# Kernel tuning notes

Measured on AMD Instinct MI355X. Metric: run time of the kernel, lower is better.

Reference implementation:

```python
import jax, jax.numpy as jnp
import numpy as np

PAD_IDX = 0
VOCAB = 60
HIDDEN = 128
BATCH = 1024
SEQ = 256


def setup_inputs() -> dict:
    key = jax.random.key(0)
    ks = jax.random.split(key, 6)
    x = jax.random.randint(ks[0], (BATCH, SEQ), 0, VOCAB, dtype=jnp.int64 if jax.config.jax_enable_x64 else jnp.int32)
    lengths = jax.random.randint(ks[1], (BATCH,), 1, SEQ + 1, dtype=x.dtype)
    emb = jax.random.normal(ks[2], (VOCAB, HIDDEN), dtype=jnp.float32) * 0.1
    emb = emb.at[PAD_IDX].set(0.0)  # nn.Embedding padding_idx row is zero
    W_ih = jax.random.normal(ks[3], (HIDDEN, HIDDEN), dtype=jnp.float32) * (1.0 / np.sqrt(HIDDEN))
    W_hh = jax.random.normal(ks[4], (HIDDEN, HIDDEN), dtype=jnp.float32) * (1.0 / np.sqrt(HIDDEN))
    W_fc = jax.random.normal(ks[5], (VOCAB, HIDDEN), dtype=jnp.float32) * (1.0 / np.sqrt(HIDDEN))
    b_fc = jnp.zeros((VOCAB,), dtype=jnp.float32)
    return {"x": x, "lengths": lengths, "emb": emb, "W_ih": W_ih,
            "W_hh": W_hh, "W_fc": W_fc, "b_fc": b_fc}


def reference(x, lengths, emb, W_ih, W_hh, W_fc, b_fc):
    embedded = emb[x]                      # [B, T, H]
    B = embedded.shape[0]
    h0 = jnp.zeros((B, HIDDEN), dtype=embedded.dtype)

    def step(h_prev, x_t):
        # z_t = x_t @ W_ih^T + h_prev @ W_hh^T ; h_t = tanh(z_t)
        h_t = jnp.tanh(x_t @ W_ih.T + h_prev @ W_hh.T)
        return h_t, h_t

    _, hs = jax.lax.scan(step, h0, jnp.swapaxes(embedded, 0, 1))  # hs: [T, B, H]
    outputs = jnp.swapaxes(hs, 0, 1)       # [B, T, H]
    last_out = jnp.take_along_axis(outputs, (lengths - 1)[:, None, None], axis=1)[:, 0, :]  # [B, H]
    return last_out @ W_fc.T + b_fc[None, :]
```

## Files before the change

kernel.cpp:

```cpp
#include <hip/hip_runtime.h>
#include <hip/hip_bf16.h>

#define BATCH 1024
#define SEQ 256
#define HIDDEN 128
#define VOCAB 60
#define ROWS 4
#define ASTRIDE 144
#define XSTR (SEQ + 4)

typedef _Float16 f16x8 __attribute__((ext_vector_type(8)));
typedef float f32x4 __attribute__((ext_vector_type(4)));

__device__ __forceinline__ float fast_tanh(float x) {
    float e = __builtin_amdgcn_exp2f(x * 2.8853900817779268f);
    return __builtin_fmaf(-2.0f, __builtin_amdgcn_rcpf(e + 1.0f), 1.0f);
}

__device__ __forceinline__ f32x4 MF(f16x8 a, f16x8 b, f32x4 c) {
    return __builtin_amdgcn_mfma_f32_16x16x32_f16(a, b, c, 0, 0, 0);
}

__global__ void rnn_prep_embw(const float* __restrict__ emb,
                              const float* __restrict__ W_ih,
                              float* __restrict__ embW) {
    const int v = blockIdx.x;
    const int i = threadIdx.x;
    __shared__ __align__(16) float e[HIDDEN];
    e[i] = emb[v * HIDDEN + i];
    __syncthreads();
    const float4* wrow = (const float4*)(W_ih + i * HIDDEN);
    const float4* e4 = (const float4*)e;
    float a0 = 0.f, a1 = 0.f, a2 = 0.f, a3 = 0.f;
#pragma unroll
    for (int j = 0; j < HIDDEN / 4; ++j) {
        float4 w = wrow[j];
        float4 h = e4[j];
        a0 += w.x * h.x; a1 += w.y * h.y; a2 += w.z * h.z; a3 += w.w * h.w;
    }
    embW[v * HIDDEN + i] = (a0 + a1) + (a2 + a3);
}

__global__ void __launch_bounds__(256)
rnn_mfma(const int* __restrict__ x, const int* __restrict__ lengths,
         const float* __restrict__ embW, const float* __restrict__ W_hh,
         const float* __restrict__ W_fc, const float* __restrict__ b_fc,
         float* __restrict__ out) {
    const int tid = threadIdx.x;
    const int wave = tid >> 6;
    const int lane = tid & 63;
    const int q = lane >> 4;
    const int r16 = lane & 15;
    const int r4 = r16 & 3;
    const int c0 = wave * 32;
    const int b0 = blockIdx.x * ROWS;

    __shared__ __align__(16) _Float16 Ah[2][ROWS][ASTRIDE];
    __shared__ __align__(16) int xs[ROWS][XSTR];
    __shared__ __align__(16) float hfin[ROWS][HIDDEN];
    __shared__ int lenbuf[ROWS];

    for (int idx = tid; idx < ROWS * SEQ; idx += 256) {
        int r = idx >> 8, t = idx & (SEQ - 1);
        xs[r][t] = x[(b0 + r) * SEQ + t];
    }
    if (tid < ROWS) lenbuf[tid] = lengths[b0 + tid];
    for (int idx = tid; idx < (int)(sizeof(Ah) / 4); idx += 256)
        ((int*)Ah)[idx] = 0;

    f16x8 Wf[2][4];
#pragma unroll
    for (int cg = 0; cg < 2; ++cg) {
        const float* wrow = W_hh + (c0 + cg * 16 + r16) * HIDDEN + q * 8;
#pragma unroll
        for (int kc = 0; kc < 4; ++kc) {
            const float* p = wrow + kc * 32;
#pragma unroll
            for (int j = 0; j < 8; ++j) Wf[cg][kc][j] = (_Float16)p[j];
        }
    }

    __syncthreads();

    const int mylen = lenbuf[r4];
    const int lenmax = max(max(lenbuf[0], lenbuf[1]), max(lenbuf[2], lenbuf[3]));

    const float* eb0 = embW + c0 + 4 * q;

    int2 tk = *(const int2*)&xs[r4][0];
    f32x4 sa0 = *(const f32x4*)(eb0 + tk.x * HIDDEN);
    f32x4 sb0 = *(const f32x4*)(eb0 + tk.x * HIDDEN + 16);
    f32x4 sa1 = *(const f32x4*)(eb0 + tk.y * HIDDEN);
    f32x4 sb1 = *(const f32x4*)(eb0 + tk.y * HIDDEN + 16);

    int cur = 0;
    f32x4 cap0 = {0.f, 0.f, 0.f, 0.f}, cap1 = {0.f, 0.f, 0.f, 0.f};

#define STEP(TT, SA, SB) do {                                              \
    const _Float16* hb = &Ah[cur][r4][q * 8];                              \
    f16x8 H0 = *(const f16x8*)(hb + 0);                                    \
    f16x8 H1 = *(const f16x8*)(hb + 32);                                   \
    f16x8 H2 = *(const f16x8*)(hb + 64);                                   \
    f16x8 H3 = *(const f16x8*)(hb + 96);                                   \
    f32x4 a0 = (SA), a1 = (SB);                                            \
    f32x4 d0 = {0.f, 0.f, 0.f, 0.f}, d1 = {0.f, 0.f, 0.f, 0.f};            \
    a0 = MF(Wf[0][0], H0, a0);  a1 = MF(Wf[1][0], H0, a1);                 \
    d0 = MF(Wf[0][2], H2, d0);  d1 = MF(Wf[1][2], H2, d1);                 \
    a0 = MF(Wf[0][1], H1, a0);  a1 = MF(Wf[1][1], H1, a1);                 \
    d0 = MF(Wf[0][3], H3, d0);  d1 = MF(Wf[1][3], H3, d1);                 \
    f32x4 z0 = a0 + d0, z1 = a1 + d1;                                      \
    f32x4 th0, th1;                                                        \
    th0[0] = fast_tanh(z0[0]); th0[1] = fast_tanh(z0[1]);                  \
    th0[2] = fast_tanh(z0[2]); th0[3] = fast_tanh(z0[3]);                  \
    th1[0] = fast_tanh(z1[0]); th1[1] = fast_tanh(z1[1]);                  \
    th1[2] = fast_tanh(z1[2]); th1[3] = fast_tanh(z1[3]);                  \
    uint2 p0, p1;                                                          \
    p0.x = __builtin_bit_cast(unsigned int, __builtin_amdgcn_cvt_pkrtz(th0[0], th0[1])); \
    p0.y = __builtin_bit_cast(unsigned int, __builtin_amdgcn_cvt_pkrtz(th0[2], th0[3])); \
    p1.x = __builtin_bit_cast(unsigned int, __builtin_amdgcn_cvt_pkrtz(th1[0], th1[1])); \
    p1.y = __builtin_bit_cast(unsigned int, __builtin_amdgcn_cvt_pkrtz(th1[2], th1[3])); \
    const int nxt = cur ^ 1;                                               \
    if (r16 < ROWS) {                  \
        *(uint2*)&Ah[nxt][r16][c0 + 4 * q] = p0;                           \
        *(uint2*)&Ah[nxt][r16][c0 + 16 + 4 * q] = p1;                      \
    }                                                                      \
    if ((TT) + 1 == mylen) { cap0 = th0; cap1 = th1; }                     \
    __syncthreads();                                                       \
    cur = nxt;                                                             \
} while (0)

    for (int t0 = 0; t0 < lenmax; t0 += 2) {
        const int tb = min(t0 + 2, SEQ - 2);
        int2 tkn = *(const int2*)&xs[r4][tb];
        f32x4 na0 = *(const f32x4*)(eb0 + tkn.x * HIDDEN);
        f32x4 nb0 = *(const f32x4*)(eb0 + tkn.x * HIDDEN + 16);
        f32x4 na1 = *(const f32x4*)(eb0 + tkn.y * HIDDEN);
        f32x4 nb1 = *(const f32x4*)(eb0 + tkn.y * HIDDEN + 16);

        STEP(t0, sa0, sb0);
        STEP(t0 + 1, sa1, sb1);

        sa0 = na0; sb0 = nb0; sa1 = na1; sb1 = nb1;
    }
#undef STEP

    if (r16 < ROWS) {
        *(f32x4*)&hfin[r16][c0 + 4 * q] = cap0;
        *(f32x4*)&hfin[r16][c0 + 16 + 4 * q] = cap1;
    }
    __syncthreads();

    for (int rc = tid; rc < ROWS * 128; rc += 256) {
        const int r = rc >> 7;
        const int c = rc & 127;
        if (c < VOCAB) {
            const float4* hv = (const float4*)hfin[r];
            const float4* wf = (const float4*)(W_fc + c * HIDDEN);
            float a0 = 0.f, a1 = 0.f, a2 = 0.f, a3 = 0.f;
#pragma unroll
            for (int j = 0; j < HIDDEN / 4; ++j) {
                float4 h = hv[j];
                float4 w = wf[j];
                a0 += h.x * w.x; a1 += h.y * w.y; a2 += h.z * w.z; a3 += h.w * w.w;
            }
            out[(b0 + r) * VOCAB + c] = (a0 + a1) + (a2 + a3) + b_fc[c];
        }
    }
}

extern "C" void kernel_launch(void* const* d_in, const int* in_sizes, int n_in,
                              void* d_out, int out_size, void* d_ws, size_t ws_size,
                              hipStream_t stream) {
    const int* x = (const int*)d_in[0];
    const int* lengths = (const int*)d_in[1];
    const float* emb = (const float*)d_in[2];
    const float* W_ih = (const float*)d_in[3];
    const float* W_hh = (const float*)d_in[4];
    const float* W_fc = (const float*)d_in[5];
    const float* b_fc = (const float*)d_in[6];
    float* out = (float*)d_out;

    float* embW = (float*)d_ws;

    rnn_prep_embw<<<VOCAB, HIDDEN, 0, stream>>>(emb, W_ih, embW);
    rnn_mfma<<<BATCH / ROWS, 256, 0, stream>>>(x, lengths, embW, W_hh, W_fc, b_fc, out);
}
```

Before: 176.7 us.

## Split hidden columns across eight waves per block and prefetch four steps

```diff
diff --git a/kernel.cpp b/kernel.cpp
--- a/kernel.cpp
+++ b/kernel.cpp
@@ -7,7 +7,7 @@
 #define VOCAB 60
 #define ROWS 4
 #define ASTRIDE 144
-#define XSTR (SEQ + 4)
+#define XSTR 260
 
 typedef _Float16 f16x8 __attribute__((ext_vector_type(8)));
 typedef float f32x4 __attribute__((ext_vector_type(4)));
@@ -41,7 +41,7 @@
     embW[v * HIDDEN + i] = (a0 + a1) + (a2 + a3);
 }
 
-__global__ void __launch_bounds__(256)
+__global__ void __launch_bounds__(512)
 rnn_mfma(const int* __restrict__ x, const int* __restrict__ lengths,
          const float* __restrict__ embW, const float* __restrict__ W_hh,
          const float* __restrict__ W_fc, const float* __restrict__ b_fc,
@@ -52,7 +52,7 @@
     const int q = lane >> 4;
     const int r16 = lane & 15;
     const int r4 = r16 & 3;
-    const int c0 = wave * 32;
+    const int c0 = wave * 16;
     const int b0 = blockIdx.x * ROWS;
 
     __shared__ __align__(16) _Float16 Ah[2][ROWS][ASTRIDE];
@@ -60,23 +60,22 @@
     __shared__ __align__(16) float hfin[ROWS][HIDDEN];
     __shared__ int lenbuf[ROWS];
 
-    for (int idx = tid; idx < ROWS * SEQ; idx += 256) {
+    for (int idx = tid; idx < ROWS * SEQ; idx += 512) {
         int r = idx >> 8, t = idx & (SEQ - 1);
         xs[r][t] = x[(b0 + r) * SEQ + t];
     }
     if (tid < ROWS) lenbuf[tid] = lengths[b0 + tid];
-    for (int idx = tid; idx < (int)(sizeof(Ah) / 4); idx += 256)
+    for (int idx = tid; idx < (int)(sizeof(Ah) / 4); idx += 512)
         ((int*)Ah)[idx] = 0;
 
-    f16x8 Wf[2][4];
-#pragma unroll
-    for (int cg = 0; cg < 2; ++cg) {
-        const float* wrow = W_hh + (c0 + cg * 16 + r16) * HIDDEN + q * 8;
+    f16x8 Wf[4];
+    {
+        const float* wrow = W_hh + (c0 + r16) * HIDDEN + q * 8;
 #pragma unroll
         for (int kc = 0; kc < 4; ++kc) {
             const float* p = wrow + kc * 32;
 #pragma unroll
-            for (int j = 0; j < 8; ++j) Wf[cg][kc][j] = (_Float16)p[j];
+            for (int j = 0; j < 8; ++j) Wf[kc][j] = (_Float16)p[j];
         }
     }
 
@@ -87,84 +86,77 @@
 
     const float* eb0 = embW + c0 + 4 * q;
 
-    int2 tk = *(const int2*)&xs[r4][0];
-    f32x4 sa0 = *(const f32x4*)(eb0 + tk.x * HIDDEN);
-    f32x4 sb0 = *(const f32x4*)(eb0 + tk.x * HIDDEN + 16);
-    f32x4 sa1 = *(const f32x4*)(eb0 + tk.y * HIDDEN);
-    f32x4 sb1 = *(const f32x4*)(eb0 + tk.y * HIDDEN + 16);
+    int4 tk = *(const int4*)&xs[r4][0];
+    f32x4 s0 = *(const f32x4*)(eb0 + tk.x * HIDDEN);
+    f32x4 s1 = *(const f32x4*)(eb0 + tk.y * HIDDEN);
+    f32x4 s2 = *(const f32x4*)(eb0 + tk.z * HIDDEN);
+    f32x4 s3 = *(const f32x4*)(eb0 + tk.w * HIDDEN);
 
     int cur = 0;
-    f32x4 cap0 = {0.f, 0.f, 0.f, 0.f}, cap1 = {0.f, 0.f, 0.f, 0.f};
+    f32x4 cap = {0.f, 0.f, 0.f, 0.f};
 
-#define STEP(TT, SA, SB) do {                                              \
+#define STEP(TT, SA) do {                                                  \
     const _Float16* hb = &Ah[cur][r4][q * 8];                              \
     f16x8 H0 = *(const f16x8*)(hb + 0);                                    \
     f16x8 H1 = *(const f16x8*)(hb + 32);                                   \
     f16x8 H2 = *(const f16x8*)(hb + 64);                                   \
     f16x8 H3 = *(const f16x8*)(hb + 96);                                   \
-    f32x4 a0 = (SA), a1 = (SB);                                            \
-    f32x4 d0 = {0.f, 0.f, 0.f, 0.f}, d1 = {0.f, 0.f, 0.f, 0.f};            \
-    a0 = MF(Wf[0][0], H0, a0);  a1 = MF(Wf[1][0], H0, a1);                 \
-    d0 = MF(Wf[0][2], H2, d0);  d1 = MF(Wf[1][2], H2, d1);                 \
-    a0 = MF(Wf[0][1], H1, a0);  a1 = MF(Wf[1][1], H1, a1);                 \
-    d0 = MF(Wf[0][3], H3, d0);  d1 = MF(Wf[1][3], H3, d1);                 \
-    f32x4 z0 = a0 + d0, z1 = a1 + d1;                                      \
-    f32x4 th0, th1;                                                        \
-    th0[0] = fast_tanh(z0[0]); th0[1] = fast_tanh(z0[1]);                  \
-    th0[2] = fast_tanh(z0[2]); th0[3] = fast_tanh(z0[3]);                  \
-    th1[0] = fast_tanh(z1[0]); th1[1] = fast_tanh(z1[1]);                  \
-    th1[2] = fast_tanh(z1[2]); th1[3] = fast_tanh(z1[3]);                  \
-    uint2 p0, p1;                                                          \
-    p0.x = __builtin_bit_cast(unsigned int, __builtin_amdgcn_cvt_pkrtz(th0[0], th0[1])); \
-    p0.y = __builtin_bit_cast(unsigned int, __builtin_amdgcn_cvt_pkrtz(th0[2], th0[3])); \
-    p1.x = __builtin_bit_cast(unsigned int, __builtin_amdgcn_cvt_pkrtz(th1[0], th1[1])); \
-    p1.y = __builtin_bit_cast(unsigned int, __builtin_amdgcn_cvt_pkrtz(th1[2], th1[3])); \
+    f32x4 a = (SA);                                                        \
+    f32x4 d = {0.f, 0.f, 0.f, 0.f};                                        \
+    a = MF(Wf[0], H0, a);                                                  \
+    d = MF(Wf[2], H2, d);                                                  \
+    a = MF(Wf[1], H1, a);                                                  \
+    d = MF(Wf[3], H3, d);                                                  \
+    f32x4 z = a + d;                                                       \
+    f32x4 th;                                                              \
+    th[0] = fast_tanh(z[0]); th[1] = fast_tanh(z[1]);                      \
+    th[2] = fast_tanh(z[2]); th[3] = fast_tanh(z[3]);                      \
+    uint2 pk;                                                              \
+    pk.x = __builtin_bit_cast(unsigned int, __builtin_amdgcn_cvt_pkrtz(th[0], th[1])); \
+    pk.y = __builtin_bit_cast(unsigned int, __builtin_amdgcn_cvt_pkrtz(th[2], th[3])); \
     const int nxt = cur ^ 1;                                               \
-    if (r16 < ROWS) {                  \
-        *(uint2*)&Ah[nxt][r16][c0 + 4 * q] = p0;                           \
-        *(uint2*)&Ah[nxt][r16][c0 + 16 + 4 * q] = p1;                      \
-    }                                                                      \
-    if ((TT) + 1 == mylen) { cap0 = th0; cap1 = th1; }                     \
+    if (r16 < ROWS)                    \
+        *(uint2*)&Ah[nxt][r16][c0 + 4 * q] = pk;                           \
+    if ((TT) + 1 == mylen) cap = th;                                       \
     __syncthreads();                                                       \
     cur = nxt;                                                             \
 } while (0)
 
-    for (int t0 = 0; t0 < lenmax; t0 += 2) {
-        const int tb = min(t0 + 2, SEQ - 2);
-        int2 tkn = *(const int2*)&xs[r4][tb];
-        f32x4 na0 = *(const f32x4*)(eb0 + tkn.x * HIDDEN);
-        f32x4 nb0 = *(const f32x4*)(eb0 + tkn.x * HIDDEN + 16);
-        f32x4 na1 = *(const f32x4*)(eb0 + tkn.y * HIDDEN);
-        f32x4 nb1 = *(const f32x4*)(eb0 + tkn.y * HIDDEN + 16);
+    for (int t0 = 0; t0 < lenmax; t0 += 4) {
+        STEP(t0, s0);
 
-        STEP(t0, sa0, sb0);
-        STEP(t0 + 1, sa1, sb1);
+        const int tb = min(t0 + 4, SEQ - 4);
+        int4 tkn = *(const int4*)&xs[r4][tb];
+        f32x4 n0 = *(const f32x4*)(eb0 + tkn.x * HIDDEN);
+        f32x4 n1 = *(const f32x4*)(eb0 + tkn.y * HIDDEN);
+        f32x4 n2 = *(const f32x4*)(eb0 + tkn.z * HIDDEN);
+        f32x4 n3 = *(const f32x4*)(eb0 + tkn.w * HIDDEN);
 
-        sa0 = na0; sb0 = nb0; sa1 = na1; sb1 = nb1;
+        if (t0 + 1 < lenmax) STEP(t0 + 1, s1);
+        if (t0 + 2 < lenmax) STEP(t0 + 2, s2);
+        if (t0 + 3 < lenmax) STEP(t0 + 3, s3);
+
+        s0 = n0; s1 = n1; s2 = n2; s3 = n3;
     }
 #undef STEP
 
-    if (r16 < ROWS) {
-        *(f32x4*)&hfin[r16][c0 + 4 * q] = cap0;
-        *(f32x4*)&hfin[r16][c0 + 16 + 4 * q] = cap1;
-    }
+    if (r16 < ROWS)
+        *(f32x4*)&hfin[r16][c0 + 4 * q] = cap;
     __syncthreads();
 
-    for (int rc = tid; rc < ROWS * 128; rc += 256) {
-        const int r = rc >> 7;
-        const int c = rc & 127;
-        if (c < VOCAB) {
-            const float4* hv = (const float4*)hfin[r];
-            const float4* wf = (const float4*)(W_fc + c * HIDDEN);
-            float a0 = 0.f, a1 = 0.f, a2 = 0.f, a3 = 0.f;
+    const int r = tid >> 7;
+    const int c = tid & 127;
+    if (c < VOCAB) {
+        const float4* hv = (const float4*)hfin[r];
+        const float4* wf = (const float4*)(W_fc + c * HIDDEN);
+        float a0 = 0.f, a1 = 0.f, a2 = 0.f, a3 = 0.f;
 #pragma unroll
-            for (int j = 0; j < HIDDEN / 4; ++j) {
-                float4 h = hv[j];
-                float4 w = wf[j];
-                a0 += h.x * w.x; a1 += h.y * w.y; a2 += h.z * w.z; a3 += h.w * w.w;
-            }
-            out[(b0 + r) * VOCAB + c] = (a0 + a1) + (a2 + a3) + b_fc[c];
+        for (int j = 0; j < HIDDEN / 4; ++j) {
+            float4 h = hv[j];
+            float4 w = wf[j];
+            a0 += h.x * w.x; a1 += h.y * w.y; a2 += h.z * w.z; a3 += h.w * w.w;
         }
+        out[(b0 + r) * VOCAB + c] = (a0 + a1) + (a2 + a3) + b_fc[c];
     }
 }
 
@@ -183,5 +175,5 @@
     float* embW = (float*)d_ws;
 
     rnn_prep_embw<<<VOCAB, HIDDEN, 0, stream>>>(emb, W_ih, embW);
-    rnn_mfma<<<BATCH / ROWS, 256, 0, stream>>>(x, lengths, embW, W_hh, W_fc, b_fc, out);
+    rnn_mfma<<<BATCH / ROWS, 512, 0, stream>>>(x, lengths, embW, W_hh, W_fc, b_fc, out);
 }
```

New measurement: 174.7 us. About the same (-1.1%).
